# Optimization experiments

Hardware: AMD Instinct MI355X
Metric: run time of the kernel (lower is better)

## Reference

```python
import jax, jax.numpy as jnp
import numpy as np

EMB_DIM = 2048
N_HEADS = 32
N_KV_HEADS = 8
HEAD_DIM = EMB_DIM // N_HEADS  # 64
N_REP = N_HEADS // N_KV_HEADS  # 4
B = 1
T = 2048


def setup_inputs() -> dict:
    key = jax.random.key(0)
    ks = jax.random.split(key, 7)
    x = jax.random.normal(ks[0], (B, T, EMB_DIM), dtype=jnp.float32)
    # RoPE tables, standard: cos/sin of shape (T, head_dim)
    inv_freq = 1.0 / (10000.0 ** (np.arange(0, HEAD_DIM, 2, dtype=np.float32) / HEAD_DIM))
    pos = np.arange(T, dtype=np.float32)
    ang = pos[:, None] * inv_freq[None, :]            # (T, head_dim/2)
    ang = np.concatenate([ang, ang], axis=-1)         # (T, head_dim)
    cos = jnp.asarray(np.cos(ang), dtype=jnp.float32)
    sin = jnp.asarray(np.sin(ang), dtype=jnp.float32)
    s = 0.02
    Wq = jax.random.normal(ks[1], (EMB_DIM, EMB_DIM), dtype=jnp.float32) * s
    Wk = jax.random.normal(ks[2], (N_KV_HEADS * HEAD_DIM, EMB_DIM), dtype=jnp.float32) * s
    Wv = jax.random.normal(ks[3], (N_KV_HEADS * HEAD_DIM, EMB_DIM), dtype=jnp.float32) * s
    Wo = jax.random.normal(ks[4], (EMB_DIM, EMB_DIM), dtype=jnp.float32) * s
    return {"x": x, "cos": cos, "sin": sin, "Wq": Wq, "Wk": Wk, "Wv": Wv, "Wo": Wo}


def apply_rope(t, cos, sin):
    # t: (b, h, T, d); cos/sin: (T, d)
    d = t.shape[-1]
    x1, x2 = t[..., : d // 2], t[..., d // 2:]
    rotated = jnp.concatenate([-x2, x1], axis=-1)
    return t * cos[None, None] + rotated * sin[None, None]


def reference(x, cos, sin, Wq, Wk, Wv, Wo):
    b, n_tok, _ = x.shape
    q = (x @ Wq.T).reshape(b, n_tok, N_HEADS, HEAD_DIM).transpose(0, 2, 1, 3)
    k = (x @ Wk.T).reshape(b, n_tok, N_KV_HEADS, HEAD_DIM).transpose(0, 2, 1, 3)
    v = (x @ Wv.T).reshape(b, n_tok, N_KV_HEADS, HEAD_DIM).transpose(0, 2, 1, 3)
    q = apply_rope(q, cos, sin)
    k = apply_rope(k, cos, sin)
    # repeat_interleave KV heads to n_heads
    k = jnp.repeat(k, N_REP, axis=1)
    v = jnp.repeat(v, N_REP, axis=1)
    scores = jnp.einsum("bhqd,bhkd->bhqk", q, k) / jnp.sqrt(jnp.float32(HEAD_DIM))
    causal = jnp.tril(jnp.ones((n_tok, n_tok), dtype=bool))
    scores = jnp.where(causal[None, None], scores, -jnp.inf)
    weights = jax.nn.softmax(scores, axis=-1)
    ctx = jnp.einsum("bhqk,bhkd->bhqd", weights, v)
    ctx = ctx.transpose(0, 2, 1, 3).reshape(b, n_tok, EMB_DIM)
    return ctx @ Wo.T
```

## Files before the change

### kernel.cpp

```cpp
#include <hip/hip_runtime.h>
#include <hip/hip_bf16.h>
#include <stdint.h>

#define EMB   2048
#define TOK   2048
#define NH    32
#define NKV   8
#define HD    64
#define QKVN  3072

typedef __attribute__((ext_vector_type(8))) short bf16x8;
typedef __attribute__((ext_vector_type(4))) float f32x4;
typedef __attribute__((ext_vector_type(16))) float f32x16;
typedef __attribute__((ext_vector_type(4))) unsigned int u32x4;

__device__ __forceinline__ void gld16(const void* g, void* l) {
  auto gp = reinterpret_cast<const int __attribute__((address_space(1)))*>(
      reinterpret_cast<uintptr_t>(g));
  auto lp = reinterpret_cast<int __attribute__((address_space(3)))*>(
      reinterpret_cast<uintptr_t>(l));
  __builtin_amdgcn_global_load_lds(gp, lp, 16, 0, 0);
}

__device__ __forceinline__ unsigned int cvtpk_bf16(float lo, float hi) {
  unsigned int r;
  asm("v_cvt_pk_bf16_f32 %0, %1, %2" : "=v"(r) : "v"(lo), "v"(hi));
  return r;
}
__device__ __forceinline__ void pl32swap(unsigned int &a, unsigned int &b) {
  asm volatile("v_permlane32_swap_b32 %0, %1" : "+v"(a), "+v"(b));
}
__device__ __forceinline__ float fexp2(float x) {
  float r;
  asm("v_exp_f32 %0, %1" : "=v"(r) : "v"(x));
  return r;
}

__global__ void cast_all(const float* __restrict__ x,  const float* __restrict__ wq,
                         const float* __restrict__ wk, const float* __restrict__ wv,
                         const float* __restrict__ wo,
                         __hip_bfloat16* __restrict__ xb,
                         __hip_bfloat16* __restrict__ wc,
                         __hip_bfloat16* __restrict__ wob) {
  const size_t M4 = (size_t)4 * 1024 * 1024;
  const size_t M1 = (size_t)1024 * 1024;
  size_t i = ((size_t)blockIdx.x * 256 + threadIdx.x) * 4;
  const float* src;
  __hip_bfloat16* dst;
  if (i < M4)                    { src = x  + i;                 dst = xb  + i; }
  else if (i < 2*M4)             { src = wq + (i - M4);          dst = wc  + (i - M4); }
  else if (i < 2*M4 + M1)        { src = wk + (i - 2*M4);        dst = wc  + M4 + (i - 2*M4); }
  else if (i < 2*M4 + 2*M1)      { src = wv + (i - 2*M4 - M1);   dst = wc  + M4 + M1 + (i - 2*M4 - M1); }
  else                           { src = wo + (i - 2*M4 - 2*M1); dst = wob + (i - 2*M4 - 2*M1); }
  float4 v = *reinterpret_cast<const float4*>(src);
  dst[0] = __float2bfloat16(v.x);
  dst[1] = __float2bfloat16(v.y);
  dst[2] = __float2bfloat16(v.z);
  dst[3] = __float2bfloat16(v.w);
}

template<int BN, typename OT>
__global__ __launch_bounds__(512) void gemm8(const __hip_bfloat16* __restrict__ A,
                                             const __hip_bfloat16* __restrict__ B,
                                             OT* __restrict__ C,
                                             int M, int N, int K) {
  constexpr int A_BYTES = 128 * 128;
  constexpr int B_BYTES = BN * 128;
  constexpr int SLOT    = A_BYTES + B_BYTES;
  constexpr int CA = 2;
  constexpr int CB = BN / 64;
  constexpr int NR = BN / 64;
  extern __shared__ char lds[];

  const int nbc = N / BN;
  const int nwg = gridDim.x;
  int bid = blockIdx.x;
  bid = (bid & 7) * (nwg >> 3) + (bid >> 3);
  const int br = bid / nbc, bc = bid % nbc;

  const int tid  = threadIdx.x;
  const int w    = tid >> 6;
  const int lane = tid & 63;
  const int wr   = w >> 2, wc = w & 3;
  const int l15  = lane & 15, lg = lane >> 4;
  const int axor = (l15 & 7) << 4;

  const __hip_bfloat16* Ag = A + (size_t)br * 128 * K;
  const __hip_bfloat16* Bg = B + (size_t)bc * BN * K;

  const int srow = lane >> 3;
  const int scol = (((lane & 7) ^ srow) << 3);

  auto stageA = [&](char* slot, int kt) {
#pragma unroll
    for (int i = 0; i < CA; ++i) {
      const int c = w * CA + i;
      gld16(Ag + (size_t)(c * 8 + srow) * K + kt + scol, slot + c * 1024);
    }
  };
  auto stageB = [&](char* slot, int kt) {
#pragma unroll
    for (int i = 0; i < CB; ++i) {
      const int c = w * CB + i;
      gld16(Bg + (size_t)(c * 8 + srow) * K + kt + scol, slot + A_BYTES + c * 1024);
    }
  };
  auto ldA = [&](const char* sa, int m, int kk) {
    return *reinterpret_cast<const bf16x8*>(
        sa + (wr * 64 + m * 16 + l15) * 128 + ((kk * 64 + lg * 16) ^ axor));
  };
  auto ldB = [&](const char* sa, int n, int kk) {
    return *reinterpret_cast<const bf16x8*>(
        sa + A_BYTES + (wc * (BN / 4) + n * 16 + l15) * 128 + ((kk * 64 + lg * 16) ^ axor));
  };

  f32x4 acc[4][NR];
#pragma unroll
  for (int m = 0; m < 4; ++m)
#pragma unroll
    for (int n = 0; n < NR; ++n) acc[m][n] = (f32x4){0.f, 0.f, 0.f, 0.f};

  const int nt = K >> 6;

  stageA(lds, 0);         stageB(lds, 0);
  stageA(lds + SLOT, 64); stageB(lds + SLOT, 64);
  if constexpr (CA + CB == 4) asm volatile("s_waitcnt vmcnt(4)" ::: "memory");
  else                        asm volatile("s_waitcnt vmcnt(5)" ::: "memory");
  __builtin_amdgcn_s_barrier();

  int slc = 0, sls = 2;
  for (int t = 0; t < nt; ++t) {
    const char* sa = lds + slc * SLOT;
    char* stg = lds + sls * SLOT;
    const bool do_stage = (t + 2) < nt;
    const int kt2 = (t + 2) << 6;

    bf16x8 afr[2][2], bfr[NR][2];
#pragma unroll
    for (int m = 0; m < 2; ++m)
#pragma unroll
      for (int kk = 0; kk < 2; ++kk) afr[m][kk] = ldA(sa, m, kk);
#pragma unroll
    for (int n = 0; n < NR; ++n)
#pragma unroll
      for (int kk = 0; kk < 2; ++kk) bfr[n][kk] = ldB(sa, n, kk);
    if (do_stage) stageA(stg, kt2);
    __builtin_amdgcn_s_barrier();
    asm volatile("s_waitcnt lgkmcnt(0)" ::: "memory");
    __builtin_amdgcn_sched_barrier(0);
    __builtin_amdgcn_s_setprio(1);
#pragma unroll
    for (int m = 0; m < 2; ++m)
#pragma unroll
      for (int n = 0; n < NR; ++n)
#pragma unroll
        for (int kk = 0; kk < 2; ++kk)
          acc[m][n] = __builtin_amdgcn_mfma_f32_16x16x32_bf16(afr[m][kk], bfr[n][kk],
                                                              acc[m][n], 0, 0, 0);
    __builtin_amdgcn_s_setprio(0);
    __builtin_amdgcn_s_barrier();

#pragma unroll
    for (int m = 0; m < 2; ++m)
#pragma unroll
      for (int kk = 0; kk < 2; ++kk) afr[m][kk] = ldA(sa, 2 + m, kk);
    if (do_stage) stageB(stg, kt2);
    __builtin_amdgcn_s_barrier();
    asm volatile("s_waitcnt lgkmcnt(0)" ::: "memory");
    __builtin_amdgcn_sched_barrier(0);
    __builtin_amdgcn_s_setprio(1);
#pragma unroll
    for (int m = 0; m < 2; ++m)
#pragma unroll
      for (int n = 0; n < NR; ++n)
#pragma unroll
        for (int kk = 0; kk < 2; ++kk)
          acc[2 + m][n] = __builtin_amdgcn_mfma_f32_16x16x32_bf16(afr[m][kk], bfr[n][kk],
                                                                  acc[2 + m][n], 0, 0, 0);
    __builtin_amdgcn_s_setprio(0);
    if (t < nt - 2) {
      if constexpr (CA + CB == 4) asm volatile("s_waitcnt vmcnt(4)" ::: "memory");
      else                        asm volatile("s_waitcnt vmcnt(5)" ::: "memory");
    } else {
      asm volatile("s_waitcnt vmcnt(0)" ::: "memory");
    }
    __builtin_amdgcn_s_barrier();

    slc = (slc == 2) ? 0 : slc + 1;
    sls = (sls == 2) ? 0 : sls + 1;
  }

  const int row0 = br * 128 + wr * 64;
  const int col0 = bc * BN + wc * (BN / 4);
#pragma unroll
  for (int m = 0; m < 4; ++m)
#pragma unroll
    for (int n = 0; n < NR; ++n)
#pragma unroll
      for (int r = 0; r < 4; ++r) {
        const size_t off = (size_t)(row0 + m * 16 + lg * 4 + r) * N + col0 + n * 16 + l15;
        if constexpr (sizeof(OT) == 4) C[off] = acc[m][n][r];
        else                           C[off] = __float2bfloat16(acc[m][n][r]);
      }
}

#define QSCALE 0.1803368801111243f

__device__ __forceinline__ size_t kq_idx(int tile_row, int t, int d) {
  return ((size_t)tile_row) * 2048 +
         ((((d >> 4) * 64) + (((d >> 3) & 1) * 32) + (t & 31)) << 3) + (d & 7);
}

__global__ void rope_cast(const __hip_bfloat16* __restrict__ qkv,
                          const float* __restrict__ cosT, const float* __restrict__ sinT,
                          __hip_bfloat16* __restrict__ Qf,
                          __hip_bfloat16* __restrict__ Kf,
                          __hip_bfloat16* __restrict__ Vf) {
  const int QP = TOK * NH * (HD / 2);
  const int KP = TOK * NKV * (HD / 2);
  int idx = blockIdx.x * 256 + threadIdx.x;
  if (idx < QP) {
    int d = idx & 31, h = (idx >> 5) & 31, t = idx >> 10;
    const __hip_bfloat16* row = qkv + (size_t)t * QKVN + h * 64;
    float x1 = __bfloat162float(row[d]), x2 = __bfloat162float(row[d + 32]);
    float o1 = (x1 * cosT[t * 64 + d]      - x2 * sinT[t * 64 + d])      * QSCALE;
    float o2 = (x2 * cosT[t * 64 + d + 32] + x1 * sinT[t * 64 + d + 32]) * QSCALE;
    const int tile_row = h * 64 + (t >> 5);
    Qf[kq_idx(tile_row, t, d)]      = __float2bfloat16(o1);
    Qf[kq_idx(tile_row, t, d + 32)] = __float2bfloat16(o2);
  } else if (idx < QP + KP) {
    int j = idx - QP;
    int d = j & 31, hk = (j >> 5) & 7, t = j >> 8;
    const __hip_bfloat16* row = qkv + (size_t)t * QKVN + 2048 + hk * 64;
    float x1 = __bfloat162float(row[d]), x2 = __bfloat162float(row[d + 32]);
    float o1 = x1 * cosT[t * 64 + d]      - x2 * sinT[t * 64 + d];
    float o2 = x2 * cosT[t * 64 + d + 32] + x1 * sinT[t * 64 + d + 32];
    const int tile_row = hk * 64 + (t >> 5);
    Kf[kq_idx(tile_row, t, d)]      = __float2bfloat16(o1);
    Kf[kq_idx(tile_row, t, d + 32)] = __float2bfloat16(o2);
  } else {
    int vj = idx - QP - KP;
    int d = vj & 63, t = (vj >> 6) & (TOK - 1), hk = vj >> 17;
    const __hip_bfloat16 v = qkv[(size_t)t * QKVN + 2560 + hk * 64 + d];
    const size_t tb = ((size_t)hk * 64 + (t >> 5)) * 2048;
    const int c = (((t >> 4) & 1) * 128) + ((d >> 5) * 64) + (((t >> 3) & 1) * 32) + (d & 31);
    Vf[tb + (c << 3) + (t & 7)] = v;
  }
}

#define MBIAS 10.0f

struct KVb { bf16x8 k0, k1, k2, k3, v00, v01, v10, v11; };

__device__ __forceinline__ void load_kv(KVb& b, const __hip_bfloat16* Kt,
                                        const __hip_bfloat16* Vt, int tile,
                                        int lane) {
  const __hip_bfloat16* Kp = Kt + (size_t)tile * 2048 + lane * 8;
  b.k0 = *reinterpret_cast<const bf16x8*>(Kp);
  b.k1 = *reinterpret_cast<const bf16x8*>(Kp + 512);
  b.k2 = *reinterpret_cast<const bf16x8*>(Kp + 1024);
  b.k3 = *reinterpret_cast<const bf16x8*>(Kp + 1536);
  const __hip_bfloat16* Vp = Vt + (size_t)tile * 2048 + lane * 8;
  b.v00 = *reinterpret_cast<const bf16x8*>(Vp);
  b.v10 = *reinterpret_cast<const bf16x8*>(Vp + 512);
  b.v01 = *reinterpret_cast<const bf16x8*>(Vp + 1024);
  b.v11 = *reinterpret_cast<const bf16x8*>(Vp + 1536);
}

__device__ __forceinline__ void compute_tile(const KVb& b, bool diag,
                                             const bf16x8 (&qf)[4],
                                             const f32x16& minit,
                                             int l31, int hi,
                                             float& mb, float& l,
                                             f32x16& oa0, f32x16& oa1) {
  __builtin_amdgcn_s_setprio(1);
  f32x16 st = __builtin_amdgcn_mfma_f32_32x32x16_bf16(b.k0, qf[0], minit, 0, 0, 0);
  st = __builtin_amdgcn_mfma_f32_32x32x16_bf16(b.k1, qf[1], st, 0, 0, 0);
  st = __builtin_amdgcn_mfma_f32_32x32x16_bf16(b.k2, qf[2], st, 0, 0, 0);
  st = __builtin_amdgcn_mfma_f32_32x32x16_bf16(b.k3, qf[3], st, 0, 0, 0);
  __builtin_amdgcn_s_setprio(0);

  float s[16];
#pragma unroll
  for (int r = 0; r < 16; ++r) s[r] = st[r];
  if (diag) {
#pragma unroll
    for (int r = 0; r < 16; ++r) {
      const int crow = (r & 3) + 8 * (r >> 2) + 4 * hi;
      s[r] = (crow <= l31) ? s[r] : -1e30f;
    }
  }
  float a0 = fmaxf(fmaxf(s[0], s[1]),  s[2]);
  float a1 = fmaxf(fmaxf(s[3], s[4]),  s[5]);
  float a2 = fmaxf(fmaxf(s[6], s[7]),  s[8]);
  float a3 = fmaxf(fmaxf(s[9], s[10]), s[11]);
  float a4 = fmaxf(fmaxf(s[12], s[13]), s[14]);
  float rmax = fmaxf(fmaxf(fmaxf(fmaxf(a0, a1), a2), fmaxf(a3, a4)), s[15]);
  rmax = fmaxf(rmax, __shfl_xor(rmax, 32));

  if (!__all(rmax <= mb + 8.0f)) {
    const float mnew = fmaxf(mb, rmax);
    const float resc = fexp2(mb - mnew);
    l *= resc;
#pragma unroll
    for (int r = 0; r < 16; ++r) { oa0[r] *= resc; oa1[r] *= resc; }
    mb = mnew;
  }

  float p[16];
  if (mb == 0.0f) {
#pragma unroll
    for (int r = 0; r < 16; ++r) p[r] = fexp2(s[r]);
  } else {
#pragma unroll
    for (int r = 0; r < 16; ++r) p[r] = fexp2(s[r] - mb);
  }
  float u0 = (p[0] + p[1]) + (p[2] + p[3]);
  float u1 = (p[4] + p[5]) + (p[6] + p[7]);
  float u2 = (p[8] + p[9]) + (p[10] + p[11]);
  float u3 = (p[12] + p[13]) + (p[14] + p[15]);
  float rsum = (u0 + u1) + (u2 + u3);
  rsum += __shfl_xor(rsum, 32);
  l += rsum;

  unsigned int wpk[8];
#pragma unroll
  for (int j = 0; j < 8; ++j) wpk[j] = cvtpk_bf16(p[2 * j], p[2 * j + 1]);

  __builtin_amdgcn_s_setprio(1);
  {
    unsigned int x0 = wpk[0], y0 = wpk[2];  pl32swap(x0, y0);
    unsigned int x1 = wpk[1], y1 = wpk[3];  pl32swap(x1, y1);
    u32x4 pw; pw[0] = x0; pw[1] = x1; pw[2] = y0; pw[3] = y1;
    bf16x8 pf = *reinterpret_cast<bf16x8*>(&pw);
    oa0 = __builtin_amdgcn_mfma_f32_32x32x16_bf16(b.v00, pf, oa0, 0, 0, 0);
    oa1 = __builtin_amdgcn_mfma_f32_32x32x16_bf16(b.v10, pf, oa1, 0, 0, 0);
  }
  {
    unsigned int x0 = wpk[4], y0 = wpk[6];  pl32swap(x0, y0);
    unsigned int x1 = wpk[5], y1 = wpk[7];  pl32swap(x1, y1);
    u32x4 pw; pw[0] = x0; pw[1] = x1; pw[2] = y0; pw[3] = y1;
    bf16x8 pf = *reinterpret_cast<bf16x8*>(&pw);
    oa0 = __builtin_amdgcn_mfma_f32_32x32x16_bf16(b.v01, pf, oa0, 0, 0, 0);
    oa1 = __builtin_amdgcn_mfma_f32_32x32x16_bf16(b.v11, pf, oa1, 0, 0, 0);
  }
  __builtin_amdgcn_s_setprio(0);
}

__global__ __launch_bounds__(128) void attn6(const __hip_bfloat16* __restrict__ Qf,
                                             const __hip_bfloat16* __restrict__ Kf,
                                             const __hip_bfloat16* __restrict__ Vf,
                                             __hip_bfloat16* __restrict__ ctx) {
  const int idx   = blockIdx.x;
  const int hk    = idx & 7;
  const int hq    = (idx >> 3) & 3;
  const int strip = 63 - (idx >> 5);
  const int h     = hk * 4 + hq;
  const int tid   = threadIdx.x;
  const int w     = tid >> 6;
  const int lane  = tid & 63;
  const int l31   = lane & 31, hi = lane >> 5;
  const int q0    = strip * 32;
  const int nt    = strip + 1;

  __shared__ unsigned int part_u[2][32][33];
  __shared__ float mlb[2][2][32];

  const __hip_bfloat16* Kt = Kf + (size_t)hk * 64 * 2048;
  const __hip_bfloat16* Vt = Vf + (size_t)hk * 64 * 2048;

  const __hip_bfloat16* Qp = Qf + ((size_t)h * 64 + strip) * 2048 + lane * 8;
  bf16x8 qf[4];
#pragma unroll
  for (int ks = 0; ks < 4; ++ks)
    qf[ks] = *reinterpret_cast<const bf16x8*>(Qp + ks * 512);

  f32x16 minit;
#pragma unroll
  for (int r = 0; r < 16; ++r) minit[r] = -MBIAS;

  f32x16 oa0, oa1;
#pragma unroll
  for (int r = 0; r < 16; ++r) { oa0[r] = 0.f; oa1[r] = 0.f; }
  float mb = 0.f, l = 0.f;

  if (w < nt) {
    KVb A, B;
    load_kv(A, Kt, Vt, w, lane);
    int t = w;
    for (;;) {
      int nx = t + 2;
      if (nx < nt) load_kv(B, Kt, Vt, nx, lane);
      compute_tile(A, t == nt - 1, qf, minit, l31, hi, mb, l, oa0, oa1);
      t = nx;
      if (t >= nt) break;
      nx = t + 2;
      if (nx < nt) load_kv(A, Kt, Vt, nx, lane);
      compute_tile(B, t == nt - 1, qf, minit, l31, hi, mb, l, oa0, oa1);
      t = nx;
      if (t >= nt) break;
    }
  }

#pragma unroll
  for (int r = 0; r < 16; ++r) {
    const int d0 = (r & 3) + 8 * (r >> 2) + 4 * hi;
    part_u[w][d0][l31] = cvtpk_bf16(oa0[r], oa1[r]);
  }
  if (hi == 0) { mlb[w][0][l31] = mb; mlb[w][1][l31] = l; }
  __syncthreads();

  const int d  = tid & 63;
  const int qg = tid >> 6;
#pragma unroll
  for (int qq = 0; qq < 16; ++qq) {
    const int q = qg * 16 + qq;
    const float m0 = mlb[0][0][q], m1 = mlb[1][0][q];
    const float M = fmaxf(m0, m1);
    const float s0 = fexp2(m0 - M), s1 = fexp2(m1 - M);
    const float L = mlb[0][1][q] * s0 + mlb[1][1][q] * s1;
    const unsigned int u0 = part_u[0][d & 31][q];
    const unsigned int u1 = part_u[1][d & 31][q];
    const unsigned int w0 = (d < 32) ? (u0 << 16) : (u0 & 0xffff0000u);
    const unsigned int w1 = (d < 32) ? (u1 << 16) : (u1 & 0xffff0000u);
    const float p0 = __uint_as_float(w0), p1 = __uint_as_float(w1);
    ctx[(size_t)(q0 + q) * EMB + h * HD + d] = __float2bfloat16((p0 * s0 + p1 * s1) / L);
  }
}

extern "C" void kernel_launch(void* const* d_in, const int* in_sizes, int n_in,
                              void* d_out, int out_size, void* d_ws, size_t ws_size,
                              hipStream_t stream) {
  const float* x    = (const float*)d_in[0];
  const float* cosT = (const float*)d_in[1];
  const float* sinT = (const float*)d_in[2];
  const float* Wq   = (const float*)d_in[3];
  const float* Wk   = (const float*)d_in[4];
  const float* Wv   = (const float*)d_in[5];
  const float* Wo   = (const float*)d_in[6];
  float* out = (float*)d_out;

  const size_t M4 = (size_t)4 * 1024 * 1024;
  const size_t M1 = (size_t)1024 * 1024;

  char* ws = (char*)d_ws;
  __hip_bfloat16* xb   = (__hip_bfloat16*)ws;
  __hip_bfloat16* Wc   = xb + M4;
  __hip_bfloat16* Wob  = Wc + (size_t)6 * M1;
  __hip_bfloat16* qkvb = Wob + M4;
  __hip_bfloat16* Qf   = qkvb + (size_t)TOK * QKVN;
  __hip_bfloat16* Kf   = Qf + (size_t)NH * TOK * HD;
  __hip_bfloat16* Vf   = Kf + (size_t)NKV * TOK * HD;
  __hip_bfloat16* ctxb = Vf + (size_t)NKV * HD * TOK;

  constexpr int SLOT192 = 128 * 128 + 192 * 128;
  constexpr int SLOT128 = 128 * 128 + 128 * 128;
  hipFuncSetAttribute(reinterpret_cast<const void*>(&gemm8<192, __hip_bfloat16>),
                      hipFuncAttributeMaxDynamicSharedMemorySize, 3 * SLOT192);
  hipFuncSetAttribute(reinterpret_cast<const void*>(&gemm8<128, float>),
                      hipFuncAttributeMaxDynamicSharedMemorySize, 3 * SLOT128);

  cast_all<<<14336, 256, 0, stream>>>(x, Wq, Wk, Wv, Wo, xb, Wc, Wob);

  gemm8<192, __hip_bfloat16><<<256, 512, 3 * SLOT192, stream>>>(xb, Wc, qkvb,
                                                                TOK, QKVN, EMB);

  rope_cast<<<14336, 256, 0, stream>>>(qkvb, cosT, sinT, Qf, Kf, Vf);

  attn6<<<64 * 32, 128, 0, stream>>>(Qf, Kf, Vf, ctxb);

  gemm8<128, float><<<256, 512, 3 * SLOT128, stream>>>(ctxb, Wob, out, TOK, EMB, EMB);
}
```

Before: 120.5 us.

## Use one wave per attention block with software-pipelined QK and softmax-PV

The attention kernel now uses a single 64-thread wave per (head, query strip) block instead of two waves that split KV tiles and merged partial results through shared memory. Within the wave, the QK MFMA for tile t+1 is issued before the softmax and PV of tile t, and a three-buffer register rotation prefetches KV two tiles ahead. This removes the cross-wave merge, its barrier and the bf16 round-trip of partial outputs. In exchange each block runs its whole KV sequence serially, with half the threads per block and higher register pressure.

```diff
diff --git a/kernel.cpp b/kernel.cpp
--- a/kernel.cpp
+++ b/kernel.cpp
@@ -267,19 +267,21 @@
   b.v11 = *reinterpret_cast<const bf16x8*>(Vp + 1536);
 }
 
-__device__ __forceinline__ void compute_tile(const KVb& b, bool diag,
-                                             const bf16x8 (&qf)[4],
-                                             const f32x16& minit,
-                                             int l31, int hi,
-                                             float& mb, float& l,
-                                             f32x16& oa0, f32x16& oa1) {
+__device__ __forceinline__ f32x16 qk_tile(const KVb& b, const bf16x8 (&qf)[4],
+                                          const f32x16& minit) {
   __builtin_amdgcn_s_setprio(1);
   f32x16 st = __builtin_amdgcn_mfma_f32_32x32x16_bf16(b.k0, qf[0], minit, 0, 0, 0);
   st = __builtin_amdgcn_mfma_f32_32x32x16_bf16(b.k1, qf[1], st, 0, 0, 0);
   st = __builtin_amdgcn_mfma_f32_32x32x16_bf16(b.k2, qf[2], st, 0, 0, 0);
   st = __builtin_amdgcn_mfma_f32_32x32x16_bf16(b.k3, qf[3], st, 0, 0, 0);
   __builtin_amdgcn_s_setprio(0);
-
+  return st;
+}
+
+__device__ __forceinline__ void sm_pv(const f32x16& st, const KVb& b, bool diag,
+                                      int l31, int hi,
+                                      float& mb, float& l,
+                                      f32x16& oa0, f32x16& oa1) {
   float s[16];
 #pragma unroll
   for (int r = 0; r < 16; ++r) s[r] = st[r];
@@ -347,24 +349,21 @@
   __builtin_amdgcn_s_setprio(0);
 }
 
-__global__ __launch_bounds__(128) void attn6(const __hip_bfloat16* __restrict__ Qf,
-                                             const __hip_bfloat16* __restrict__ Kf,
-                                             const __hip_bfloat16* __restrict__ Vf,
-                                             __hip_bfloat16* __restrict__ ctx) {
+__global__ __launch_bounds__(64) void attnp(const __hip_bfloat16* __restrict__ Qf,
+                                            const __hip_bfloat16* __restrict__ Kf,
+                                            const __hip_bfloat16* __restrict__ Vf,
+                                            __hip_bfloat16* __restrict__ ctx) {
   const int idx   = blockIdx.x;
   const int hk    = idx & 7;
   const int hq    = (idx >> 3) & 3;
   const int strip = 63 - (idx >> 5);
   const int h     = hk * 4 + hq;
-  const int tid   = threadIdx.x;
-  const int w     = tid >> 6;
-  const int lane  = tid & 63;
+  const int lane  = threadIdx.x;
   const int l31   = lane & 31, hi = lane >> 5;
   const int q0    = strip * 32;
   const int nt    = strip + 1;
 
-  __shared__ unsigned int part_u[2][32][33];
-  __shared__ float mlb[2][2][32];
+  __shared__ float T[64][33];
 
   const __hip_bfloat16* Kt = Kf + (size_t)hk * 64 * 2048;
   const __hip_bfloat16* Vt = Vf + (size_t)hk * 64 * 2048;
@@ -384,47 +383,41 @@
   for (int r = 0; r < 16; ++r) { oa0[r] = 0.f; oa1[r] = 0.f; }
   float mb = 0.f, l = 0.f;
 
-  if (w < nt) {
-    KVb A, B;
-    load_kv(A, Kt, Vt, w, lane);
-    int t = w;
-    for (;;) {
-      int nx = t + 2;
-      if (nx < nt) load_kv(B, Kt, Vt, nx, lane);
-      compute_tile(A, t == nt - 1, qf, minit, l31, hi, mb, l, oa0, oa1);
-      t = nx;
-      if (t >= nt) break;
-      nx = t + 2;
-      if (nx < nt) load_kv(A, Kt, Vt, nx, lane);
-      compute_tile(B, t == nt - 1, qf, minit, l31, hi, mb, l, oa0, oa1);
-      t = nx;
-      if (t >= nt) break;
-    }
-  }
-
+  KVb b0, b1, b2;
+  load_kv(b0, Kt, Vt, 0, lane);
+  if (nt > 1) load_kv(b1, Kt, Vt, 1, lane);
+  f32x16 st = qk_tile(b0, qf, minit);
+  f32x16 stn;
+  int t = 0;
+  for (;;) {
+    if (t + 2 < nt) load_kv(b2, Kt, Vt, t + 2, lane);
+    if (t + 1 < nt) stn = qk_tile(b1, qf, minit);
+    sm_pv(st, b0, t == nt - 1, l31, hi, mb, l, oa0, oa1);
+    if (++t == nt) break;
+    st = stn;
+    if (t + 2 < nt) load_kv(b0, Kt, Vt, t + 2, lane);
+    if (t + 1 < nt) stn = qk_tile(b2, qf, minit);
+    sm_pv(st, b1, t == nt - 1, l31, hi, mb, l, oa0, oa1);
+    if (++t == nt) break;
+    st = stn;
+    if (t + 2 < nt) load_kv(b1, Kt, Vt, t + 2, lane);
+    if (t + 1 < nt) stn = qk_tile(b0, qf, minit);
+    sm_pv(st, b2, t == nt - 1, l31, hi, mb, l, oa0, oa1);
+    if (++t == nt) break;
+    st = stn;
+  }
+
+  const float inv = 1.f / l;
 #pragma unroll
   for (int r = 0; r < 16; ++r) {
-    const int d0 = (r & 3) + 8 * (r >> 2) + 4 * hi;
-    part_u[w][d0][l31] = cvtpk_bf16(oa0[r], oa1[r]);
-  }
-  if (hi == 0) { mlb[w][0][l31] = mb; mlb[w][1][l31] = l; }
-  __syncthreads();
-
-  const int d  = tid & 63;
-  const int qg = tid >> 6;
-#pragma unroll
-  for (int qq = 0; qq < 16; ++qq) {
-    const int q = qg * 16 + qq;
-    const float m0 = mlb[0][0][q], m1 = mlb[1][0][q];
-    const float M = fmaxf(m0, m1);
-    const float s0 = fexp2(m0 - M), s1 = fexp2(m1 - M);
-    const float L = mlb[0][1][q] * s0 + mlb[1][1][q] * s1;
-    const unsigned int u0 = part_u[0][d & 31][q];
-    const unsigned int u1 = part_u[1][d & 31][q];
-    const unsigned int w0 = (d < 32) ? (u0 << 16) : (u0 & 0xffff0000u);
-    const unsigned int w1 = (d < 32) ? (u1 << 16) : (u1 & 0xffff0000u);
-    const float p0 = __uint_as_float(w0), p1 = __uint_as_float(w1);
-    ctx[(size_t)(q0 + q) * EMB + h * HD + d] = __float2bfloat16((p0 * s0 + p1 * s1) / L);
+    const int d = (r & 3) + 8 * (r >> 2) + 4 * hi;
+    T[d][l31]      = oa0[r] * inv;
+    T[d + 32][l31] = oa1[r] * inv;
+  }
+#pragma unroll 4
+  for (int i = 0; i < 32; ++i) {
+    const float v = T[lane][i];
+    ctx[(size_t)(q0 + i) * EMB + h * HD + lane] = __float2bfloat16(v);
   }
 }
 
@@ -467,7 +460,7 @@
 
   rope_cast<<<14336, 256, 0, stream>>>(qkvb, cosT, sinT, Qf, Kf, Vf);
 
-  attn6<<<64 * 32, 128, 0, stream>>>(Qf, Kf, Vf, ctxb);
+  attnp<<<64 * 32, 64, 0, stream>>>(Qf, Kf, Vf, ctxb);
 
   gemm8<128, float><<<256, 512, 3 * SLOT128, stream>>>(ctxb, Wob, out, TOK, EMB, EMB);
 }
```

Result: slower. 136.8 us (+13.6%).

## Share K/V tiles across GQA query heads via LDS in attention kernel

Applied to the files above, without the earlier changes.

The attention kernel is restructured so each block handles all four query heads that share one KV head. There are 8 waves: 4 heads times 2 tile parities. K/V tiles are staged once into double-buffered LDS using global_load_lds and read by all four head waves, instead of each wave loading K/V from global memory into registers on its own. This cuts redundant K/V global traffic by about 4x. In exchange it adds a block-wide barrier every iteration, uses more LDS, and launches a quarter as many blocks, which could reduce latency hiding or occupancy.

```diff
diff --git a/kernel.cpp b/kernel.cpp
--- a/kernel.cpp
+++ b/kernel.cpp
@@ -250,121 +250,26 @@
 
 #define MBIAS 10.0f
 
-struct KVb { bf16x8 k0, k1, k2, k3, v00, v01, v10, v11; };
-
-__device__ __forceinline__ void load_kv(KVb& b, const __hip_bfloat16* Kt,
-                                        const __hip_bfloat16* Vt, int tile,
-                                        int lane) {
-  const __hip_bfloat16* Kp = Kt + (size_t)tile * 2048 + lane * 8;
-  b.k0 = *reinterpret_cast<const bf16x8*>(Kp);
-  b.k1 = *reinterpret_cast<const bf16x8*>(Kp + 512);
-  b.k2 = *reinterpret_cast<const bf16x8*>(Kp + 1024);
-  b.k3 = *reinterpret_cast<const bf16x8*>(Kp + 1536);
-  const __hip_bfloat16* Vp = Vt + (size_t)tile * 2048 + lane * 8;
-  b.v00 = *reinterpret_cast<const bf16x8*>(Vp);
-  b.v10 = *reinterpret_cast<const bf16x8*>(Vp + 512);
-  b.v01 = *reinterpret_cast<const bf16x8*>(Vp + 1024);
-  b.v11 = *reinterpret_cast<const bf16x8*>(Vp + 1536);
-}
-
-__device__ __forceinline__ void compute_tile(const KVb& b, bool diag,
-                                             const bf16x8 (&qf)[4],
-                                             const f32x16& minit,
-                                             int l31, int hi,
-                                             float& mb, float& l,
-                                             f32x16& oa0, f32x16& oa1) {
-  __builtin_amdgcn_s_setprio(1);
-  f32x16 st = __builtin_amdgcn_mfma_f32_32x32x16_bf16(b.k0, qf[0], minit, 0, 0, 0);
-  st = __builtin_amdgcn_mfma_f32_32x32x16_bf16(b.k1, qf[1], st, 0, 0, 0);
-  st = __builtin_amdgcn_mfma_f32_32x32x16_bf16(b.k2, qf[2], st, 0, 0, 0);
-  st = __builtin_amdgcn_mfma_f32_32x32x16_bf16(b.k3, qf[3], st, 0, 0, 0);
-  __builtin_amdgcn_s_setprio(0);
-
-  float s[16];
-#pragma unroll
-  for (int r = 0; r < 16; ++r) s[r] = st[r];
-  if (diag) {
-#pragma unroll
-    for (int r = 0; r < 16; ++r) {
-      const int crow = (r & 3) + 8 * (r >> 2) + 4 * hi;
-      s[r] = (crow <= l31) ? s[r] : -1e30f;
-    }
-  }
-  float a0 = fmaxf(fmaxf(s[0], s[1]),  s[2]);
-  float a1 = fmaxf(fmaxf(s[3], s[4]),  s[5]);
-  float a2 = fmaxf(fmaxf(s[6], s[7]),  s[8]);
-  float a3 = fmaxf(fmaxf(s[9], s[10]), s[11]);
-  float a4 = fmaxf(fmaxf(s[12], s[13]), s[14]);
-  float rmax = fmaxf(fmaxf(fmaxf(fmaxf(a0, a1), a2), fmaxf(a3, a4)), s[15]);
-  rmax = fmaxf(rmax, __shfl_xor(rmax, 32));
-
-  if (!__all(rmax <= mb + 8.0f)) {
-    const float mnew = fmaxf(mb, rmax);
-    const float resc = fexp2(mb - mnew);
-    l *= resc;
-#pragma unroll
-    for (int r = 0; r < 16; ++r) { oa0[r] *= resc; oa1[r] *= resc; }
-    mb = mnew;
-  }
-
-  float p[16];
-  if (mb == 0.0f) {
-#pragma unroll
-    for (int r = 0; r < 16; ++r) p[r] = fexp2(s[r]);
-  } else {
-#pragma unroll
-    for (int r = 0; r < 16; ++r) p[r] = fexp2(s[r] - mb);
-  }
-  float u0 = (p[0] + p[1]) + (p[2] + p[3]);
-  float u1 = (p[4] + p[5]) + (p[6] + p[7]);
-  float u2 = (p[8] + p[9]) + (p[10] + p[11]);
-  float u3 = (p[12] + p[13]) + (p[14] + p[15]);
-  float rsum = (u0 + u1) + (u2 + u3);
-  rsum += __shfl_xor(rsum, 32);
-  l += rsum;
-
-  unsigned int wpk[8];
-#pragma unroll
-  for (int j = 0; j < 8; ++j) wpk[j] = cvtpk_bf16(p[2 * j], p[2 * j + 1]);
-
-  __builtin_amdgcn_s_setprio(1);
-  {
-    unsigned int x0 = wpk[0], y0 = wpk[2];  pl32swap(x0, y0);
-    unsigned int x1 = wpk[1], y1 = wpk[3];  pl32swap(x1, y1);
-    u32x4 pw; pw[0] = x0; pw[1] = x1; pw[2] = y0; pw[3] = y1;
-    bf16x8 pf = *reinterpret_cast<bf16x8*>(&pw);
-    oa0 = __builtin_amdgcn_mfma_f32_32x32x16_bf16(b.v00, pf, oa0, 0, 0, 0);
-    oa1 = __builtin_amdgcn_mfma_f32_32x32x16_bf16(b.v10, pf, oa1, 0, 0, 0);
-  }
-  {
-    unsigned int x0 = wpk[4], y0 = wpk[6];  pl32swap(x0, y0);
-    unsigned int x1 = wpk[5], y1 = wpk[7];  pl32swap(x1, y1);
-    u32x4 pw; pw[0] = x0; pw[1] = x1; pw[2] = y0; pw[3] = y1;
-    bf16x8 pf = *reinterpret_cast<bf16x8*>(&pw);
-    oa0 = __builtin_amdgcn_mfma_f32_32x32x16_bf16(b.v01, pf, oa0, 0, 0, 0);
-    oa1 = __builtin_amdgcn_mfma_f32_32x32x16_bf16(b.v11, pf, oa1, 0, 0, 0);
-  }
-  __builtin_amdgcn_s_setprio(0);
-}
-
-__global__ __launch_bounds__(128) void attn6(const __hip_bfloat16* __restrict__ Qf,
-                                             const __hip_bfloat16* __restrict__ Kf,
-                                             const __hip_bfloat16* __restrict__ Vf,
-                                             __hip_bfloat16* __restrict__ ctx) {
+__global__ __launch_bounds__(512, 4) void attnL(const __hip_bfloat16* __restrict__ Qf,
+                                                const __hip_bfloat16* __restrict__ Kf,
+                                                const __hip_bfloat16* __restrict__ Vf,
+                                                __hip_bfloat16* __restrict__ ctx) {
   const int idx   = blockIdx.x;
   const int hk    = idx & 7;
-  const int hq    = (idx >> 3) & 3;
-  const int strip = 63 - (idx >> 5);
-  const int h     = hk * 4 + hq;
+  const int strip = 63 - (idx >> 3);
   const int tid   = threadIdx.x;
   const int w     = tid >> 6;
   const int lane  = tid & 63;
   const int l31   = lane & 31, hi = lane >> 5;
+  const int hq    = w & 3;
+  const int pr    = w >> 2;
+  const int h     = hk * 4 + hq;
   const int q0    = strip * 32;
-  const int nt    = strip + 1;
-
-  __shared__ unsigned int part_u[2][32][33];
-  __shared__ float mlb[2][2][32];
+  const int niter = (strip >> 1) + 1;
+
+  __shared__ char kv[2][16384];
+  __shared__ unsigned int part_u[8][32][33];
+  __shared__ float mlb[8][2][32];
 
   const __hip_bfloat16* Kt = Kf + (size_t)hk * 64 * 2048;
   const __hip_bfloat16* Vt = Vf + (size_t)hk * 64 * 2048;
@@ -384,22 +289,112 @@
   for (int r = 0; r < 16; ++r) { oa0[r] = 0.f; oa1[r] = 0.f; }
   float mb = 0.f, l = 0.f;
 
-  if (w < nt) {
-    KVb A, B;
-    load_kv(A, Kt, Vt, w, lane);
-    int t = w;
-    for (;;) {
-      int nx = t + 2;
-      if (nx < nt) load_kv(B, Kt, Vt, nx, lane);
-      compute_tile(A, t == nt - 1, qf, minit, l31, hi, mb, l, oa0, oa1);
-      t = nx;
-      if (t >= nt) break;
-      nx = t + 2;
-      if (nx < nt) load_kv(A, Kt, Vt, nx, lane);
-      compute_tile(B, t == nt - 1, qf, minit, l31, hi, mb, l, oa0, oa1);
-      t = nx;
-      if (t >= nt) break;
+  const int sseg = w >> 1, shh = w & 1;
+  const __hip_bfloat16* sbase = (sseg < 2) ? Kt : Vt;
+  auto stage_pair = [&](int buf, int it) {
+    const int tt = 2 * it + (sseg & 1);
+    const int tc = (tt <= strip) ? tt : strip;
+    const __hip_bfloat16* src = sbase + (size_t)tc * 2048 + shh * 1024 + lane * 8;
+    char* dst = &kv[buf][((sseg >= 2) ? 8192 : 0) + (sseg & 1) * 4096 + shh * 2048];
+    gld16(src,       dst);
+    gld16(src + 512, dst + 1024);
+  };
+
+  stage_pair(0, 0);
+  __syncthreads();
+
+  for (int it = 0; it < niter; ++it) {
+    if (it + 1 < niter) stage_pair((it + 1) & 1, it + 1);
+
+    const int t = 2 * it + pr;
+    if (t <= strip) {
+      const char* kb = &kv[it & 1][pr * 4096];
+      const char* vb = &kv[it & 1][8192 + pr * 4096];
+      const int lo = lane * 16;
+      const bf16x8 k0 = *reinterpret_cast<const bf16x8*>(kb + lo);
+      const bf16x8 k1 = *reinterpret_cast<const bf16x8*>(kb + 1024 + lo);
+      const bf16x8 k2 = *reinterpret_cast<const bf16x8*>(kb + 2048 + lo);
+      const bf16x8 k3 = *reinterpret_cast<const bf16x8*>(kb + 3072 + lo);
+
+      __builtin_amdgcn_s_setprio(1);
+      f32x16 st = __builtin_amdgcn_mfma_f32_32x32x16_bf16(k0, qf[0], minit, 0, 0, 0);
+      st = __builtin_amdgcn_mfma_f32_32x32x16_bf16(k1, qf[1], st, 0, 0, 0);
+      st = __builtin_amdgcn_mfma_f32_32x32x16_bf16(k2, qf[2], st, 0, 0, 0);
+      st = __builtin_amdgcn_mfma_f32_32x32x16_bf16(k3, qf[3], st, 0, 0, 0);
+      __builtin_amdgcn_s_setprio(0);
+
+      float s[16];
+#pragma unroll
+      for (int r = 0; r < 16; ++r) s[r] = st[r];
+      if (t == strip) {
+#pragma unroll
+        for (int r = 0; r < 16; ++r) {
+          const int crow = (r & 3) + 8 * (r >> 2) + 4 * hi;
+          s[r] = (crow <= l31) ? s[r] : -1e30f;
+        }
+      }
+      float a0 = fmaxf(fmaxf(s[0], s[1]),  s[2]);
+      float a1 = fmaxf(fmaxf(s[3], s[4]),  s[5]);
+      float a2 = fmaxf(fmaxf(s[6], s[7]),  s[8]);
+      float a3 = fmaxf(fmaxf(s[9], s[10]), s[11]);
+      float a4 = fmaxf(fmaxf(s[12], s[13]), s[14]);
+      float rmax = fmaxf(fmaxf(fmaxf(fmaxf(a0, a1), a2), fmaxf(a3, a4)), s[15]);
+      rmax = fmaxf(rmax, __shfl_xor(rmax, 32));
+
+      if (!__all(rmax <= mb + 8.0f)) {
+        const float mnew = fmaxf(mb, rmax);
+        const float resc = fexp2(mb - mnew);
+        l *= resc;
+#pragma unroll
+        for (int r = 0; r < 16; ++r) { oa0[r] *= resc; oa1[r] *= resc; }
+        mb = mnew;
+      }
+
+      float p[16];
+      if (mb == 0.0f) {
+#pragma unroll
+        for (int r = 0; r < 16; ++r) p[r] = fexp2(s[r]);
+      } else {
+#pragma unroll
+        for (int r = 0; r < 16; ++r) p[r] = fexp2(s[r] - mb);
+      }
+      float u0 = (p[0] + p[1]) + (p[2] + p[3]);
+      float u1 = (p[4] + p[5]) + (p[6] + p[7]);
+      float u2 = (p[8] + p[9]) + (p[10] + p[11]);
+      float u3 = (p[12] + p[13]) + (p[14] + p[15]);
+      float rsum = (u0 + u1) + (u2 + u3);
+      rsum += __shfl_xor(rsum, 32);
+      l += rsum;
+
+      unsigned int wpk[8];
+#pragma unroll
+      for (int j = 0; j < 8; ++j) wpk[j] = cvtpk_bf16(p[2 * j], p[2 * j + 1]);
+
+      const bf16x8 v00 = *reinterpret_cast<const bf16x8*>(vb + lo);
+      const bf16x8 v10 = *reinterpret_cast<const bf16x8*>(vb + 1024 + lo);
+      const bf16x8 v01 = *reinterpret_cast<const bf16x8*>(vb + 2048 + lo);
+      const bf16x8 v11 = *reinterpret_cast<const bf16x8*>(vb + 3072 + lo);
+
+      __builtin_amdgcn_s_setprio(1);
+      {
+        unsigned int x0 = wpk[0], y0 = wpk[2];  pl32swap(x0, y0);
+        unsigned int x1 = wpk[1], y1 = wpk[3];  pl32swap(x1, y1);
+        u32x4 pw; pw[0] = x0; pw[1] = x1; pw[2] = y0; pw[3] = y1;
+        bf16x8 pf = *reinterpret_cast<bf16x8*>(&pw);
+        oa0 = __builtin_amdgcn_mfma_f32_32x32x16_bf16(v00, pf, oa0, 0, 0, 0);
+        oa1 = __builtin_amdgcn_mfma_f32_32x32x16_bf16(v10, pf, oa1, 0, 0, 0);
+      }
+      {
+        unsigned int x0 = wpk[4], y0 = wpk[6];  pl32swap(x0, y0);
+        unsigned int x1 = wpk[5], y1 = wpk[7];  pl32swap(x1, y1);
+        u32x4 pw; pw[0] = x0; pw[1] = x1; pw[2] = y0; pw[3] = y1;
+        bf16x8 pf = *reinterpret_cast<bf16x8*>(&pw);
+        oa0 = __builtin_amdgcn_mfma_f32_32x32x16_bf16(v01, pf, oa0, 0, 0, 0);
+        oa1 = __builtin_amdgcn_mfma_f32_32x32x16_bf16(v11, pf, oa1, 0, 0, 0);
+      }
+      __builtin_amdgcn_s_setprio(0);
     }
+    __syncthreads();
   }
 
 #pragma unroll
@@ -411,20 +406,23 @@
   __syncthreads();
 
   const int d  = tid & 63;
-  const int qg = tid >> 6;
+  const int g  = tid >> 6;
+  const int mh = g & 3, qh = g >> 2;
+  const int w0 = mh, w1 = mh + 4;
 #pragma unroll
   for (int qq = 0; qq < 16; ++qq) {
-    const int q = qg * 16 + qq;
-    const float m0 = mlb[0][0][q], m1 = mlb[1][0][q];
+    const int q = qh * 16 + qq;
+    const float m0 = mlb[w0][0][q], m1 = mlb[w1][0][q];
     const float M = fmaxf(m0, m1);
     const float s0 = fexp2(m0 - M), s1 = fexp2(m1 - M);
-    const float L = mlb[0][1][q] * s0 + mlb[1][1][q] * s1;
-    const unsigned int u0 = part_u[0][d & 31][q];
-    const unsigned int u1 = part_u[1][d & 31][q];
-    const unsigned int w0 = (d < 32) ? (u0 << 16) : (u0 & 0xffff0000u);
-    const unsigned int w1 = (d < 32) ? (u1 << 16) : (u1 & 0xffff0000u);
-    const float p0 = __uint_as_float(w0), p1 = __uint_as_float(w1);
-    ctx[(size_t)(q0 + q) * EMB + h * HD + d] = __float2bfloat16((p0 * s0 + p1 * s1) / L);
+    const float L = mlb[w0][1][q] * s0 + mlb[w1][1][q] * s1;
+    const unsigned int u0 = part_u[w0][d & 31][q];
+    const unsigned int u1 = part_u[w1][d & 31][q];
+    const unsigned int b0 = (d < 32) ? (u0 << 16) : (u0 & 0xffff0000u);
+    const unsigned int b1 = (d < 32) ? (u1 << 16) : (u1 & 0xffff0000u);
+    const float p0 = __uint_as_float(b0), p1 = __uint_as_float(b1);
+    ctx[(size_t)(q0 + q) * EMB + (hk * 4 + mh) * HD + d] =
+        __float2bfloat16((p0 * s0 + p1 * s1) / L);
   }
 }
 
@@ -467,7 +465,7 @@
 
   rope_cast<<<14336, 256, 0, stream>>>(qkvb, cosT, sinT, Qf, Kf, Vf);
 
-  attn6<<<64 * 32, 128, 0, stream>>>(Qf, Kf, Vf, ctxb);
+  attnL<<<64 * 8, 512, 0, stream>>>(Qf, Kf, Vf, ctxb);
 
   gemm8<128, float><<<256, 512, 3 * SLOT128, stream>>>(ctxb, Wob, out, TOK, EMB, EMB);
 }
```

Measured after the change: 122.2 us. No clear change (+1.4%).
